# Kernel tuning notes

Hardware: AMD Instinct MI355X
Metric: run time of the kernel (lower is better)

The kernel has to match this reference:

```python
import jax, jax.numpy as jnp
import numpy as np

B, C, H, W = 4, 64, 64, 64
C8 = C // 8


def cl_attention(x, gamma):
    # DANet CAM-style channel attention: [B,C,H,W] -> [B,C,H,W]
    b, c, h, w = x.shape
    xf = x.reshape(b, c, h * w)                       # b c n
    energy = jnp.einsum('bcn,bdn->bcd', xf, xf)       # b c c
    energy = jnp.max(energy, axis=-1, keepdims=True) - energy
    attn = jax.nn.softmax(energy, axis=-1)
    out = jnp.einsum('bcd,bdn->bcn', attn, xf).reshape(b, c, h, w)
    return gamma * out + x


def setup_inputs() -> dict:
    key = jax.random.key(0)
    ks = jax.random.split(key, 8)
    s = 0.02
    return {
        'cnn_feat': jax.random.normal(ks[0], (B, C, H, W), jnp.float32),
        'vit_feat': jax.random.normal(ks[1], (B, C, H, W), jnp.float32),
        'Wq': jax.random.normal(ks[2], (C8, C), jnp.float32) * s,   # 1x1 conv kernel
        'bq': jnp.zeros((C8,), jnp.float32),
        'Wk': jax.random.normal(ks[3], (C8, C), jnp.float32) * s,
        'bk': jnp.zeros((C8,), jnp.float32),
        'Wv': jax.random.normal(ks[4], (C, C), jnp.float32) * s,
        'bv': jnp.zeros((C,), jnp.float32),
        'gamma': jnp.zeros((1,), jnp.float32),
        'gamma_cla_cnn': jnp.zeros((1,), jnp.float32),
        'gamma_cla_vit': jnp.zeros((1,), jnp.float32),
    }


def reference(cnn_feat, vit_feat, Wq, bq, Wk, bk, Wv, bv, gamma,
              gamma_cla_cnn, gamma_cla_vit):
    b, c, h, w = cnn_feat.shape
    n = h * w

    cnn_att = cl_attention(cnn_feat, gamma_cla_cnn)   # b c h w
    vit_att = cl_attention(vit_feat, gamma_cla_vit)   # b c h w

    # query: 1x1 conv -> view(b, C8, n) -> permute -> (b, n, C8)
    q = jnp.einsum('bchw,oc->bhwo', cnn_att, Wq).reshape(b, n, -1) + bq

    # vit: rearrange 'b c h w -> b (h w) c'
    vit_flat = vit_att.reshape(b, c, n).transpose(0, 2, 1)          # b n c
    k = vit_flat @ Wk.T + bk                                        # b n C8
    v = vit_flat @ Wv.T + bv                                        # b n C

    energy = jnp.einsum('bqd,bkd->bqk', q, k)                       # b n n
    attn = jax.nn.softmax(energy, axis=-1)
    out = jnp.einsum('bqk,bkc->bqc', attn, v)                       # b n c
    out = out.transpose(0, 2, 1).reshape(b, c, h, w)                # 'b (h w) c -> b c h w'
    return gamma * out + cnn_feat
```

## Files before the change

kernel.cpp:

```cpp
#include <hip/hip_runtime.h>
#include <hip/hip_bf16.h>

#define BSZ 4
#define CC 64
#define NN 4096
#define CN (CC*NN)
#define BCN (BSZ*CN)

typedef __attribute__((ext_vector_type(4))) float    f4v;
typedef __attribute__((ext_vector_type(4))) int      i4v;
typedef __attribute__((ext_vector_type(2))) int      i2v;
typedef __attribute__((ext_vector_type(2))) unsigned u2v;
typedef __attribute__((ext_vector_type(8))) short    s8v;

#define DPP_F(x_, ctrl_) __builtin_bit_cast(float, \
    __builtin_amdgcn_update_dpp(0, __builtin_bit_cast(int, (float)(x_)), (ctrl_), 0xf, 0xf, true))
#define QP_X1 0xB1

__device__ __forceinline__ unsigned pack_bf16(float lo, float hi) {
    unsigned l = __builtin_bit_cast(unsigned, lo);
    unsigned h = __builtin_bit_cast(unsigned, hi);
    return (h & 0xFFFF0000u) | (l >> 16);
}
__device__ __forceinline__ unsigned pack2(float lo, float hi) {
    float2 f2; f2.x = lo; f2.y = hi;
    __hip_bfloat162 h = __float22bfloat162_rn(f2);
    unsigned u;
    __builtin_memcpy(&u, &h, 4);
    return u;
}
__device__ __forceinline__ float blo(int d) {
    return __builtin_bit_cast(float, (unsigned)d << 16);
}
__device__ __forceinline__ float bhi(int d) {
    return __builtin_bit_cast(float, (unsigned)d & 0xFFFF0000u);
}

__global__ __launch_bounds__(256) void gram_k(const float* __restrict__ cnn,
                                              const float* __restrict__ vit,
                                              float* __restrict__ part) {
    __shared__ __align__(16) float sXT[128*68];
    int t = threadIdx.x;
    int blk = blockIdx.x;
    int ch = blk & 31, b = (blk >> 5) & 3, i2 = blk >> 7;
    const float* X = (i2 ? vit : cnn) + b * CN;
    int n0 = ch * 128;
#pragma unroll
    for (int j = 0; j < 8; j++) {
        int idx = t + j * 256;
        int c = idx >> 5, n4 = idx & 31;
        f4v val = *(const f4v*)&X[c * NN + n0 + n4 * 4];
        int base = (n4 * 4) * 68 + c;
        sXT[base]       = val[0];
        sXT[base + 68]  = val[1];
        sXT[base + 136] = val[2];
        sXT[base + 204] = val[3];
    }
    __syncthreads();
    int tc = (t & 15) * 4, td = (t >> 4) * 4;
    f4v acc[4];
#pragma unroll
    for (int i = 0; i < 4; i++) acc[i] = (f4v){0.f, 0.f, 0.f, 0.f};
#pragma unroll 4
    for (int k = 0; k < 128; k++) {
        f4v a  = *(const f4v*)&sXT[k * 68 + tc];
        f4v bb = *(const f4v*)&sXT[k * 68 + td];
#pragma unroll
        for (int i = 0; i < 4; i++) acc[i] += a[i] * bb;
    }
    float* dst = part + ch * 32768 + (i2 * 4 + b) * 4096;
#pragma unroll
    for (int i = 0; i < 4; i++) *(f4v*)&dst[(tc + i) * 64 + td] = acc[i];
}

__global__ void gred_k(const float* __restrict__ part, float* __restrict__ G) {
    int row = blockIdx.x;
    int d = threadIdx.x;
    float s = 0.f;
#pragma unroll 8
    for (int ch = 0; ch < 32; ch++) s += part[ch * 32768 + row * 64 + d];
    float mn = s;
#pragma unroll
    for (int off = 1; off < 64; off <<= 1) mn = fminf(mn, __shfl_xor(mn, off));
    float e = __expf(mn - s);
    float sm = e;
#pragma unroll
    for (int off = 1; off < 64; off <<= 1) sm += __shfl_xor(sm, off);
    G[row * 64 + d] = e / sm;
}

__global__ __launch_bounds__(256) void weff_k(const float* __restrict__ G,
                                              const float* __restrict__ Wq,
                                              const float* __restrict__ Wk,
                                              const float* __restrict__ Wv,
                                              const float* __restrict__ gcnn,
                                              const float* __restrict__ gvit,
                                              ushort* __restrict__ WeffB) {
    __shared__ float sA[8192];
    __shared__ float sWt[1024];
    int t = threadIdx.x;
    int b = blockIdx.x / 5, tile = blockIdx.x % 5;
    for (int i = t; i < 4096; i += 256) {
        sA[i]        = G[b * 4096 + i];
        sA[4096 + i] = G[(4 + b) * 4096 + i];
    }
    __syncthreads();
    float gc = *gcnn, gv = *gvit;
#pragma unroll
    for (int k = 0; k < 4; k++) {
        int idx = k * 256 + t;
        int r = idx >> 6, c = idx & 63;
        const float* Wrow; const float* A; float g;
        if (tile == 0) {
            if (r < 8) { Wrow = Wq + r * 64;       A = sA;        g = gc; }
            else       { Wrow = Wk + (r - 8) * 64; A = sA + 4096; g = gv; }
        } else         { Wrow = Wv + ((tile - 1) * 16 + r) * 64; A = sA + 4096; g = gv; }
        float s = 0.f;
#pragma unroll 8
        for (int d = 0; d < 64; d++) s += Wrow[d] * A[d * 64 + c];
        sWt[idx] = g * s + Wrow[c];
    }
    __syncthreads();
    if (t < 128) {
        int frag = t >> 6, lane = t & 63, m = lane & 15, q4 = lane >> 4;
        i4v o;
#pragma unroll
        for (int p = 0; p < 4; p++) {
            int c0 = frag * 32 + q4 * 8 + 2 * p;
            o[p] = (int)pack_bf16(sWt[m * 64 + c0], sWt[m * 64 + c0 + 1]);
        }
        *(i4v*)&WeffB[(size_t)(b * 10 + tile * 2 + frag) * 512 + lane * 8] = o;
    }
}

__global__ __launch_bounds__(256) void qkv_k(const float* __restrict__ cnn,
                                             const float* __restrict__ vit,
                                             const ushort* __restrict__ WeffB,
                                             const float* __restrict__ bq,
                                             const float* __restrict__ bk,
                                             const float* __restrict__ bv,
                                             ushort* __restrict__ qb, ushort* __restrict__ kb,
                                             ushort* __restrict__ vT) {
    int t = threadIdx.x;
    int b = blockIdx.x >> 6, n0 = (blockIdx.x & 63) * 64;
    int w = t >> 6, lane = t & 63, c15 = lane & 15, q4 = lane >> 4;
    int n = n0 + w * 16 + c15;
    const float LOG2E = 1.44269504f;

    s8v A[10];
    const ushort* WB = WeffB + (size_t)b * 5120 + lane * 8;
#pragma unroll
    for (int i = 0; i < 10; i++)
        A[i] = __builtin_bit_cast(s8v, *(const i4v*)(WB + (size_t)i * 512));

    s8v Bc[2], Bv[2];
#pragma unroll
    for (int f = 0; f < 2; f++) {
        i4v pc, pv;
#pragma unroll
        for (int p = 0; p < 4; p++) {
            int c0 = f * 32 + q4 * 8 + p * 2;
            size_t a0 = (size_t)b * CN + (size_t)c0 * NN + n;
            pc[p] = (int)pack_bf16(cnn[a0], cnn[a0 + NN]);
            pv[p] = (int)pack_bf16(vit[a0], vit[a0 + NN]);
        }
        Bc[f] = __builtin_bit_cast(s8v, pc);
        Bv[f] = __builtin_bit_cast(s8v, pv);
    }

    f4v acc = *(const f4v*)(bq + (q4 & 1) * 4);
    acc = __builtin_amdgcn_mfma_f32_16x16x32_bf16(A[0], Bc[0], acc, 0, 0, 0);
    acc = __builtin_amdgcn_mfma_f32_16x16x32_bf16(A[1], Bc[1], acc, 0, 0, 0);
    if (q4 < 2) {
        unsigned d0 = pack_bf16(acc[0] * LOG2E, acc[1] * LOG2E);
        unsigned d1 = pack_bf16(acc[2] * LOG2E, acc[3] * LOG2E);
        unsigned long long v = ((unsigned long long)d1 << 32) | d0;
        *(unsigned long long*)&qb[(size_t)(b * NN + n) * 8 + q4 * 4] = v;
    }
    acc = *(const f4v*)(bk + (q4 & 1) * 4);
    acc = __builtin_amdgcn_mfma_f32_16x16x32_bf16(A[0], Bv[0], acc, 0, 0, 0);
    acc = __builtin_amdgcn_mfma_f32_16x16x32_bf16(A[1], Bv[1], acc, 0, 0, 0);
    if (q4 >= 2) {
        unsigned d0 = pack_bf16(acc[0], acc[1]), d1 = pack_bf16(acc[2], acc[3]);
        unsigned long long v = ((unsigned long long)d1 << 32) | d0;
        *(unsigned long long*)&kb[(size_t)(b * NN + n) * 8 + (q4 - 2) * 4] = v;
    }
#pragma unroll
    for (int tile = 1; tile < 5; tile++) {
        acc = *(const f4v*)(bv + (tile - 1) * 16 + q4 * 4);
        acc = __builtin_amdgcn_mfma_f32_16x16x32_bf16(A[tile * 2],     Bv[0], acc, 0, 0, 0);
        acc = __builtin_amdgcn_mfma_f32_16x16x32_bf16(A[tile * 2 + 1], Bv[1], acc, 0, 0, 0);
#pragma unroll
        for (int r = 0; r < 4; r++) {
            float other = DPP_F(acc[r], QP_X1);
            unsigned pkd = (lane & 1) ? pack_bf16(other, acc[r])
                                      : pack_bf16(acc[r], other);
            if (!(lane & 1)) {
                int row = (tile - 1) * 16 + q4 * 4 + r;
                *(unsigned*)&vT[(size_t)(b * 64 + row) * NN + n] = pkd;
            }
        }
    }
}

__global__ __launch_bounds__(256, 2) void flash_k(const ushort* __restrict__ qb,
                                                  const ushort* __restrict__ kb,
                                                  const ushort* __restrict__ vT,
                                                  ushort* __restrict__ pOT,
                                                  float* __restrict__ pl) {
    __shared__ __align__(16) ushort Vlds[2 * 64 * 72];
    int t = threadIdx.x;
    int lane = t & 63, w = t >> 6;
    int c15 = lane & 15, q4 = lane >> 4;
    int blk = blockIdx.x;
    int s = blk >> 7, b = (blk >> 5) & 3, q0 = (blk & 31) * 128;

    s8v qB[2];
#pragma unroll
    for (int g = 0; g < 2; g++) {
        i4v qa = (i4v){0, 0, 0, 0};
        if (q4 == 0)
            qa = *(const i4v*)(qb + (size_t)(b * NN + q0 + w * 32 + g * 16 + c15) * 8);
        qB[g] = __builtin_bit_cast(s8v, qa);
    }

    f4v accO[2][4];
#pragma unroll
    for (int g = 0; g < 2; g++)
#pragma unroll
        for (int nt = 0; nt < 4; nt++) accO[g][nt] = (f4v){0.f, 0.f, 0.f, 0.f};
    float lacc[2] = {0.f, 0.f};

    const ushort* kbb = kb + (size_t)b * NN * 8 + (size_t)c15 * 8;

    int r = t >> 2, chk = t & 3;
    const ushort* vsrc = vT + (size_t)(b * 64 + r) * NN + chk * 16;
    int vdstoff = r * 72 + 32 * (chk >> 1) + 4 * (chk & 1);
    int vreadoff = c15 * 72 + 8 * q4;

    int kbase = s * 1024;
    i4v bk_cur[4];
#pragma unroll
    for (int nt = 0; nt < 4; nt++)
        bk_cur[nt] = *(const i4v*)(kbb + (size_t)(kbase + nt * 16) * 8);
    i4v v0 = *(const i4v*)(vsrc + kbase);
    i4v v1 = *(const i4v*)(vsrc + kbase + 8);

#pragma unroll 2
    for (int kt = 0; kt < 16; kt++) {
        int k0 = kbase + kt * 64;
        ushort* vd = Vlds + (kt & 1) * 4608 + vdstoff;
        *(i2v*)(vd + 0)  = (i2v){v0[0], v0[1]};
        *(i2v*)(vd + 8)  = (i2v){v0[2], v0[3]};
        *(i2v*)(vd + 16) = (i2v){v1[0], v1[1]};
        *(i2v*)(vd + 24) = (i2v){v1[2], v1[3]};
        __syncthreads();

        const ushort* vb = Vlds + (kt & 1) * 4608 + vreadoff;
        i4v vA[2][4];
#pragma unroll
        for (int F = 0; F < 2; F++)
#pragma unroll
            for (int nt = 0; nt < 4; nt++)
                vA[F][nt] = *(const i4v*)(vb + nt * 16 * 72 + 32 * F);

        i4v bk_nxt[4];
        if (kt < 15) {
            v0 = *(const i4v*)(vsrc + k0 + 64);
            v1 = *(const i4v*)(vsrc + k0 + 64 + 8);
#pragma unroll
            for (int nt = 0; nt < 4; nt++)
                bk_nxt[nt] = *(const i4v*)(kbb + (size_t)(k0 + 64 + nt * 16) * 8);
        }

        f4v z = (f4v){0.f, 0.f, 0.f, 0.f};
        f4v S[2][4];
#pragma unroll
        for (int g = 0; g < 2; g++)
#pragma unroll
            for (int nt = 0; nt < 4; nt++)
                S[g][nt] = __builtin_amdgcn_mfma_f32_16x16x32_bf16(
                    __builtin_bit_cast(s8v, bk_cur[nt]), qB[g], z, 0, 0, 0);

        s8v Bp[2][2];
#pragma unroll
        for (int g = 0; g < 2; g++) {
            f4v p[4];
            float ps = 0.f;
#pragma unroll
            for (int nt = 0; nt < 4; nt++)
#pragma unroll
                for (int rr = 0; rr < 4; rr++) {
                    p[nt][rr] = __builtin_amdgcn_exp2f(S[g][nt][rr]);
                    ps += p[nt][rr];
                }
#pragma unroll
            for (int F = 0; F < 2; F++) {
                i4v bp;
                bp[0] = (int)pack2(p[2 * F][0],     p[2 * F][1]);
                bp[1] = (int)pack2(p[2 * F][2],     p[2 * F][3]);
                bp[2] = (int)pack2(p[2 * F + 1][0], p[2 * F + 1][1]);
                bp[3] = (int)pack2(p[2 * F + 1][2], p[2 * F + 1][3]);
                Bp[g][F] = __builtin_bit_cast(s8v, bp);
            }
            lacc[g] += ps;
        }

        __builtin_amdgcn_s_setprio(1);
#pragma unroll
        for (int F = 0; F < 2; F++)
#pragma unroll
            for (int g = 0; g < 2; g++)
#pragma unroll
                for (int nt = 0; nt < 4; nt++)
                    accO[g][nt] =
                        __builtin_amdgcn_mfma_f32_16x16x32_bf16(
                            __builtin_bit_cast(s8v, vA[F][nt]), Bp[g][F],
                            accO[g][nt], 0, 0, 0);
        __builtin_amdgcn_s_setprio(0);

        if (kt < 15) {
#pragma unroll
            for (int nt = 0; nt < 4; nt++) bk_cur[nt] = bk_nxt[nt];
        }
    }

#pragma unroll
    for (int g = 0; g < 2; g++) {
        lacc[g] += __shfl_xor(lacc[g], 16);
        lacc[g] += __shfl_xor(lacc[g], 32);
    }

#pragma unroll
    for (int g = 0; g < 2; g++) {
        int qg = q0 + w * 32 + g * 16 + c15;
#pragma unroll
        for (int nt = 0; nt < 4; nt++) {
            int cg = nt * 4 + q4;
            u2v d;
            d[0] = pack2(accO[g][nt][0], accO[g][nt][1]);
            d[1] = pack2(accO[g][nt][2], accO[g][nt][3]);
            *(u2v*)&pOT[((size_t)((s * 4 + b) * 16 + cg) * NN + qg) * 4] = d;
        }
        if (q4 == 0)
            pl[(size_t)(s * 4 + b) * NN + qg] = lacc[g];
    }
}

__global__ __launch_bounds__(256) void comb_k(const ushort* __restrict__ pOT,
                                              const float* __restrict__ pl,
                                              const float* __restrict__ cnn,
                                              const float* __restrict__ gamma,
                                              float* __restrict__ out) {
    int t = threadIdx.x;
    int b = blockIdx.x >> 6, n0 = (blockIdx.x & 63) * 64;
    int nq = t & 15, cl = t >> 4;
    int n = n0 + nq * 4;
    f4v L = (f4v){0.f, 0.f, 0.f, 0.f};
#pragma unroll
    for (int s = 0; s < 4; s++)
        L += *(const f4v*)&pl[(size_t)(s * 4 + b) * NN + n];
    float g = *gamma;
    f4v rv;
#pragma unroll
    for (int j = 0; j < 4; j++) rv[j] = g / L[j];

    f4v Oc[4];
#pragma unroll
    for (int cc = 0; cc < 4; cc++) Oc[cc] = (f4v){0.f, 0.f, 0.f, 0.f};
#pragma unroll
    for (int s = 0; s < 4; s++) {
        const ushort* src = pOT + ((size_t)((s * 4 + b) * 16 + cl) * NN + n) * 4;
        i4v a  = *(const i4v*)src;
        i4v bb = *(const i4v*)(src + 8);
        Oc[0][0] += blo(a[0]);  Oc[1][0] += bhi(a[0]);
        Oc[2][0] += blo(a[1]);  Oc[3][0] += bhi(a[1]);
        Oc[0][1] += blo(a[2]);  Oc[1][1] += bhi(a[2]);
        Oc[2][1] += blo(a[3]);  Oc[3][1] += bhi(a[3]);
        Oc[0][2] += blo(bb[0]); Oc[1][2] += bhi(bb[0]);
        Oc[2][2] += blo(bb[1]); Oc[3][2] += bhi(bb[1]);
        Oc[0][3] += blo(bb[2]); Oc[1][3] += bhi(bb[2]);
        Oc[2][3] += blo(bb[3]); Oc[3][3] += bhi(bb[3]);
    }
#pragma unroll
    for (int cc = 0; cc < 4; cc++) {
        size_t gi = (size_t)(b * 64 + cl * 4 + cc) * NN + n;
        f4v cv = *(const f4v*)&cnn[gi];
        *(f4v*)&out[gi] = Oc[cc] * rv + cv;
    }
}

extern "C" void kernel_launch(void* const* d_in, const int* in_sizes, int n_in,
                              void* d_out, int out_size, void* d_ws, size_t ws_size,
                              hipStream_t stream) {
    const float* cnn  = (const float*)d_in[0];
    const float* vit  = (const float*)d_in[1];
    const float* Wq   = (const float*)d_in[2];
    const float* bq   = (const float*)d_in[3];
    const float* Wk   = (const float*)d_in[4];
    const float* bk   = (const float*)d_in[5];
    const float* Wv   = (const float*)d_in[6];
    const float* bv   = (const float*)d_in[7];
    const float* gam  = (const float*)d_in[8];
    const float* gcnn = (const float*)d_in[9];
    const float* gvit = (const float*)d_in[10];
    float* out = (float*)d_out;

    float* ws = (float*)d_ws;
    ushort* pOT   = (ushort*)ws;
    float*  part  = ws;
    float*  G     = ws + 8388608;
    ushort* WeffB = (ushort*)(ws + 8421376);
    ushort* qb    = (ushort*)(ws + 8431616);
    ushort* kb    = (ushort*)(ws + 8497152);
    ushort* vT    = (ushort*)(ws + 8562688);
    float*  pl    = ws + 9086976;

    gram_k <<<256, 256, 0, stream>>>(cnn, vit, part);
    gred_k <<<512, 64,  0, stream>>>(part, G);
    weff_k <<<20,  256, 0, stream>>>(G, Wq, Wk, Wv, gcnn, gvit, WeffB);
    qkv_k  <<<256, 256, 0, stream>>>(cnn, vit, WeffB, bq, bk, bv, qb, kb, vT);
    flash_k<<<512, 256, 0, stream>>>(qb, kb, vT, pOT, pl);
    comb_k <<<256, 256, 0, stream>>>(pOT, pl, cnn, gam, out);
}
```

Before: 126.6 us.

## Fuse split-K combine into flash kernel with in-block LDS reduction and prepacked V fragments

Drops the separate combine kernel and the bf16 partial-output and denominator buffers. Each block now handles 64 queries, and its four waves each cover a quarter of the keys. The waves reduce their partial outputs and softmax denominators through shared memory, then apply gamma and the residual add directly. qkv_k now writes V in MFMA-fragment order, so flashB loads V fragments straight from global memory with no LDS staging or per-iteration barriers. The cost is half as many blocks (256), more registers per wave for the larger accumulator set, and a multi-step LDS reduction at the end.

```diff
diff --git a/kernel.cpp b/kernel.cpp
--- a/kernel.cpp
+++ b/kernel.cpp
@@ -10,12 +10,7 @@
 typedef __attribute__((ext_vector_type(4))) float    f4v;
 typedef __attribute__((ext_vector_type(4))) int      i4v;
 typedef __attribute__((ext_vector_type(2))) int      i2v;
-typedef __attribute__((ext_vector_type(2))) unsigned u2v;
 typedef __attribute__((ext_vector_type(8))) short    s8v;
-
-#define DPP_F(x_, ctrl_) __builtin_bit_cast(float, \
-    __builtin_amdgcn_update_dpp(0, __builtin_bit_cast(int, (float)(x_)), (ctrl_), 0xf, 0xf, true))
-#define QP_X1 0xB1
 
 __device__ __forceinline__ unsigned pack_bf16(float lo, float hi) {
     unsigned l = __builtin_bit_cast(unsigned, lo);
@@ -28,12 +23,6 @@
     unsigned u;
     __builtin_memcpy(&u, &h, 4);
     return u;
-}
-__device__ __forceinline__ float blo(int d) {
-    return __builtin_bit_cast(float, (unsigned)d << 16);
-}
-__device__ __forceinline__ float bhi(int d) {
-    return __builtin_bit_cast(float, (unsigned)d & 0xFFFF0000u);
 }
 
 __global__ __launch_bounds__(256) void gram_k(const float* __restrict__ cnn,
@@ -140,9 +129,10 @@
                                              const float* __restrict__ bk,
                                              const float* __restrict__ bv,
                                              ushort* __restrict__ qb, ushort* __restrict__ kb,
-                                             ushort* __restrict__ vT) {
+                                             ushort* __restrict__ vF) {
+    __shared__ float vbuf[64 * 67];
     int t = threadIdx.x;
-    int b = blockIdx.x >> 6, n0 = (blockIdx.x & 63) * 64;
+    int b = blockIdx.x >> 6, ktg = blockIdx.x & 63, n0 = ktg * 64;
     int w = t >> 6, lane = t & 63, c15 = lane & 15, q4 = lane >> 4;
     int n = n0 + w * 16 + c15;
     const float LOG2E = 1.44269504f;
@@ -191,109 +181,104 @@
         acc = __builtin_amdgcn_mfma_f32_16x16x32_bf16(A[tile * 2],     Bv[0], acc, 0, 0, 0);
         acc = __builtin_amdgcn_mfma_f32_16x16x32_bf16(A[tile * 2 + 1], Bv[1], acc, 0, 0, 0);
 #pragma unroll
-        for (int r = 0; r < 4; r++) {
-            float other = DPP_F(acc[r], QP_X1);
-            unsigned pkd = (lane & 1) ? pack_bf16(other, acc[r])
-                                      : pack_bf16(acc[r], other);
-            if (!(lane & 1)) {
-                int row = (tile - 1) * 16 + q4 * 4 + r;
-                *(unsigned*)&vT[(size_t)(b * 64 + row) * NN + n] = pkd;
-            }
-        }
-    }
-}
-
-__global__ __launch_bounds__(256, 2) void flash_k(const ushort* __restrict__ qb,
-                                                  const ushort* __restrict__ kb,
-                                                  const ushort* __restrict__ vT,
-                                                  ushort* __restrict__ pOT,
-                                                  float* __restrict__ pl) {
-    __shared__ __align__(16) ushort Vlds[2 * 64 * 72];
+        for (int r = 0; r < 4; r++)
+            vbuf[((tile - 1) * 16 + q4 * 4 + r) * 67 + w * 16 + c15] = acc[r];
+    }
+    __syncthreads();
+    {
+        int nt = w, l = lane, q4f = q4, c15f = c15;
+#pragma unroll
+        for (int F = 0; F < 2; F++) {
+            float vv[8];
+#pragma unroll
+            for (int e = 0; e < 8; e++)
+                vv[e] = vbuf[(nt * 16 + c15f) * 67 + 32 * F + 16 * (e >> 2)
+                             + 4 * q4f + (e & 3)];
+            i4v o;
+#pragma unroll
+            for (int p = 0; p < 4; p++)
+                o[p] = (int)pack_bf16(vv[2 * p], vv[2 * p + 1]);
+            *(i4v*)&vF[((size_t)((b * 64 + ktg) * 8 + nt * 2 + F)) * 512 + l * 8] = o;
+        }
+    }
+}
+
+__global__ __launch_bounds__(256, 2) void flashB(
+        const ushort* __restrict__ qb, const ushort* __restrict__ kb,
+        const ushort* __restrict__ vF, const float* __restrict__ cnn,
+        const float* __restrict__ gamma, float* __restrict__ out) {
+    __shared__ __align__(16) float sO[2][64 * 68];
+    __shared__ float sL[4][64];
+    __shared__ float sRv[64];
+
     int t = threadIdx.x;
     int lane = t & 63, w = t >> 6;
     int c15 = lane & 15, q4 = lane >> 4;
     int blk = blockIdx.x;
-    int s = blk >> 7, b = (blk >> 5) & 3, q0 = (blk & 31) * 128;
-
-    s8v qB[2];
-#pragma unroll
-    for (int g = 0; g < 2; g++) {
+    int b = blk >> 6, q0 = (blk & 63) * 64;
+    float gm = *gamma;
+
+    s8v qB[4];
+#pragma unroll
+    for (int g = 0; g < 4; g++) {
         i4v qa = (i4v){0, 0, 0, 0};
         if (q4 == 0)
-            qa = *(const i4v*)(qb + (size_t)(b * NN + q0 + w * 32 + g * 16 + c15) * 8);
+            qa = *(const i4v*)(qb + (size_t)(b * NN + q0 + g * 16 + c15) * 8);
         qB[g] = __builtin_bit_cast(s8v, qa);
     }
 
-    f4v accO[2][4];
-#pragma unroll
-    for (int g = 0; g < 2; g++)
+    f4v accO[4][4];
+#pragma unroll
+    for (int g = 0; g < 4; g++)
 #pragma unroll
         for (int nt = 0; nt < 4; nt++) accO[g][nt] = (f4v){0.f, 0.f, 0.f, 0.f};
-    float lacc[2] = {0.f, 0.f};
+    float lacc[4] = {0.f, 0.f, 0.f, 0.f};
 
     const ushort* kbb = kb + (size_t)b * NN * 8 + (size_t)c15 * 8;
-
-    int r = t >> 2, chk = t & 3;
-    const ushort* vsrc = vT + (size_t)(b * 64 + r) * NN + chk * 16;
-    int vdstoff = r * 72 + 32 * (chk >> 1) + 4 * (chk & 1);
-    int vreadoff = c15 * 72 + 8 * q4;
-
-    int kbase = s * 1024;
-    i4v bk_cur[4];
+    const ushort* vfb = vF + (size_t)b * 64 * 8 * 512 + (size_t)lane * 8;
+    int kq = w * 1024;
+
+    i4v bkc[4];
 #pragma unroll
     for (int nt = 0; nt < 4; nt++)
-        bk_cur[nt] = *(const i4v*)(kbb + (size_t)(kbase + nt * 16) * 8);
-    i4v v0 = *(const i4v*)(vsrc + kbase);
-    i4v v1 = *(const i4v*)(vsrc + kbase + 8);
-
-#pragma unroll 2
+        bkc[nt] = *(const i4v*)(kbb + (size_t)(kq + nt * 16) * 8);
+
     for (int kt = 0; kt < 16; kt++) {
-        int k0 = kbase + kt * 64;
-        ushort* vd = Vlds + (kt & 1) * 4608 + vdstoff;
-        *(i2v*)(vd + 0)  = (i2v){v0[0], v0[1]};
-        *(i2v*)(vd + 8)  = (i2v){v0[2], v0[3]};
-        *(i2v*)(vd + 16) = (i2v){v1[0], v1[1]};
-        *(i2v*)(vd + 24) = (i2v){v1[2], v1[3]};
-        __syncthreads();
-
-        const ushort* vb = Vlds + (kt & 1) * 4608 + vreadoff;
+        int ktg = (kq >> 6) + kt;
         i4v vA[2][4];
 #pragma unroll
         for (int F = 0; F < 2; F++)
 #pragma unroll
             for (int nt = 0; nt < 4; nt++)
-                vA[F][nt] = *(const i4v*)(vb + nt * 16 * 72 + 32 * F);
-
-        i4v bk_nxt[4];
+                vA[F][nt] = *(const i4v*)(vfb +
+                    (size_t)(ktg * 8 + nt * 2 + F) * 512);
+        i4v bkn[4];
         if (kt < 15) {
-            v0 = *(const i4v*)(vsrc + k0 + 64);
-            v1 = *(const i4v*)(vsrc + k0 + 64 + 8);
-#pragma unroll
-            for (int nt = 0; nt < 4; nt++)
-                bk_nxt[nt] = *(const i4v*)(kbb + (size_t)(k0 + 64 + nt * 16) * 8);
-        }
-
-        f4v z = (f4v){0.f, 0.f, 0.f, 0.f};
-        f4v S[2][4];
-#pragma unroll
-        for (int g = 0; g < 2; g++)
-#pragma unroll
-            for (int nt = 0; nt < 4; nt++)
-                S[g][nt] = __builtin_amdgcn_mfma_f32_16x16x32_bf16(
-                    __builtin_bit_cast(s8v, bk_cur[nt]), qB[g], z, 0, 0, 0);
-
-        s8v Bp[2][2];
-#pragma unroll
-        for (int g = 0; g < 2; g++) {
+#pragma unroll
+            for (int nt = 0; nt < 4; nt++)
+                bkn[nt] = *(const i4v*)(kbb +
+                    (size_t)(kq + (kt + 1) * 64 + nt * 16) * 8);
+        }
+
+#pragma unroll
+        for (int g = 0; g < 4; g++) {
+            f4v z = (f4v){0.f, 0.f, 0.f, 0.f};
+            f4v S[4];
+#pragma unroll
+            for (int nt = 0; nt < 4; nt++)
+                S[nt] = __builtin_amdgcn_mfma_f32_16x16x32_bf16(
+                    __builtin_bit_cast(s8v, bkc[nt]), qB[g], z, 0, 0, 0);
             f4v p[4];
             float ps = 0.f;
 #pragma unroll
             for (int nt = 0; nt < 4; nt++)
 #pragma unroll
                 for (int rr = 0; rr < 4; rr++) {
-                    p[nt][rr] = __builtin_amdgcn_exp2f(S[g][nt][rr]);
+                    p[nt][rr] = __builtin_amdgcn_exp2f(S[nt][rr]);
                     ps += p[nt][rr];
                 }
+            lacc[g] += ps;
+            s8v Bp[2];
 #pragma unroll
             for (int F = 0; F < 2; F++) {
                 i4v bp;
@@ -301,92 +286,88 @@
                 bp[1] = (int)pack2(p[2 * F][2],     p[2 * F][3]);
                 bp[2] = (int)pack2(p[2 * F + 1][0], p[2 * F + 1][1]);
                 bp[3] = (int)pack2(p[2 * F + 1][2], p[2 * F + 1][3]);
-                Bp[g][F] = __builtin_bit_cast(s8v, bp);
+                Bp[F] = __builtin_bit_cast(s8v, bp);
             }
-            lacc[g] += ps;
-        }
-
-        __builtin_amdgcn_s_setprio(1);
-#pragma unroll
-        for (int F = 0; F < 2; F++)
-#pragma unroll
-            for (int g = 0; g < 2; g++)
+            __builtin_amdgcn_s_setprio(1);
+#pragma unroll
+            for (int F = 0; F < 2; F++)
 #pragma unroll
                 for (int nt = 0; nt < 4; nt++)
-                    accO[g][nt] =
-                        __builtin_amdgcn_mfma_f32_16x16x32_bf16(
-                            __builtin_bit_cast(s8v, vA[F][nt]), Bp[g][F],
-                            accO[g][nt], 0, 0, 0);
-        __builtin_amdgcn_s_setprio(0);
-
+                    accO[g][nt] = __builtin_amdgcn_mfma_f32_16x16x32_bf16(
+                        __builtin_bit_cast(s8v, vA[F][nt]), Bp[F],
+                        accO[g][nt], 0, 0, 0);
+            __builtin_amdgcn_s_setprio(0);
+        }
         if (kt < 15) {
 #pragma unroll
-            for (int nt = 0; nt < 4; nt++) bk_cur[nt] = bk_nxt[nt];
-        }
-    }
-
-#pragma unroll
-    for (int g = 0; g < 2; g++) {
+            for (int nt = 0; nt < 4; nt++) bkc[nt] = bkn[nt];
+        }
+    }
+
+#pragma unroll
+    for (int g = 0; g < 4; g++) {
         lacc[g] += __shfl_xor(lacc[g], 16);
         lacc[g] += __shfl_xor(lacc[g], 32);
-    }
-
-#pragma unroll
-    for (int g = 0; g < 2; g++) {
-        int qg = q0 + w * 32 + g * 16 + c15;
-#pragma unroll
-        for (int nt = 0; nt < 4; nt++) {
-            int cg = nt * 4 + q4;
-            u2v d;
-            d[0] = pack2(accO[g][nt][0], accO[g][nt][1]);
-            d[1] = pack2(accO[g][nt][2], accO[g][nt][3]);
-            *(u2v*)&pOT[((size_t)((s * 4 + b) * 16 + cg) * NN + qg) * 4] = d;
-        }
-        if (q4 == 0)
-            pl[(size_t)(s * 4 + b) * NN + qg] = lacc[g];
-    }
-}
-
-__global__ __launch_bounds__(256) void comb_k(const ushort* __restrict__ pOT,
-                                              const float* __restrict__ pl,
-                                              const float* __restrict__ cnn,
-                                              const float* __restrict__ gamma,
-                                              float* __restrict__ out) {
-    int t = threadIdx.x;
-    int b = blockIdx.x >> 6, n0 = (blockIdx.x & 63) * 64;
-    int nq = t & 15, cl = t >> 4;
-    int n = n0 + nq * 4;
-    f4v L = (f4v){0.f, 0.f, 0.f, 0.f};
-#pragma unroll
-    for (int s = 0; s < 4; s++)
-        L += *(const f4v*)&pl[(size_t)(s * 4 + b) * NN + n];
-    float g = *gamma;
-    f4v rv;
-#pragma unroll
-    for (int j = 0; j < 4; j++) rv[j] = g / L[j];
-
-    f4v Oc[4];
-#pragma unroll
-    for (int cc = 0; cc < 4; cc++) Oc[cc] = (f4v){0.f, 0.f, 0.f, 0.f};
-#pragma unroll
-    for (int s = 0; s < 4; s++) {
-        const ushort* src = pOT + ((size_t)((s * 4 + b) * 16 + cl) * NN + n) * 4;
-        i4v a  = *(const i4v*)src;
-        i4v bb = *(const i4v*)(src + 8);
-        Oc[0][0] += blo(a[0]);  Oc[1][0] += bhi(a[0]);
-        Oc[2][0] += blo(a[1]);  Oc[3][0] += bhi(a[1]);
-        Oc[0][1] += blo(a[2]);  Oc[1][1] += bhi(a[2]);
-        Oc[2][1] += blo(a[3]);  Oc[3][1] += bhi(a[3]);
-        Oc[0][2] += blo(bb[0]); Oc[1][2] += bhi(bb[0]);
-        Oc[2][2] += blo(bb[1]); Oc[3][2] += bhi(bb[1]);
-        Oc[0][3] += blo(bb[2]); Oc[1][3] += bhi(bb[2]);
-        Oc[2][3] += blo(bb[3]); Oc[3][3] += bhi(bb[3]);
-    }
-#pragma unroll
-    for (int cc = 0; cc < 4; cc++) {
-        size_t gi = (size_t)(b * 64 + cl * 4 + cc) * NN + n;
+        if (q4 == 0) sL[w][g * 16 + c15] = lacc[g];
+    }
+    if (w >= 2) {
+        float* s = sO[w - 2];
+#pragma unroll
+        for (int g = 0; g < 4; g++)
+#pragma unroll
+            for (int nt = 0; nt < 4; nt++)
+#pragma unroll
+                for (int rr = 0; rr < 4; rr++)
+                    s[(nt * 16 + q4 * 4 + rr) * 68 + g * 16 + c15] = accO[g][nt][rr];
+    }
+    __syncthreads();
+    if (w < 2) {
+        float* s = sO[w];
+#pragma unroll
+        for (int g = 0; g < 4; g++)
+#pragma unroll
+            for (int nt = 0; nt < 4; nt++)
+#pragma unroll
+                for (int rr = 0; rr < 4; rr++)
+                    accO[g][nt][rr] += s[(nt * 16 + q4 * 4 + rr) * 68 + g * 16 + c15];
+    }
+    if (w == 1) {
+        float* s = sO[1];
+#pragma unroll
+        for (int g = 0; g < 4; g++)
+#pragma unroll
+            for (int nt = 0; nt < 4; nt++)
+#pragma unroll
+                for (int rr = 0; rr < 4; rr++)
+                    s[(nt * 16 + q4 * 4 + rr) * 68 + g * 16 + c15] = accO[g][nt][rr];
+    }
+    if (w == 2) {
+        float Ls = sL[0][lane] + sL[1][lane] + sL[2][lane] + sL[3][lane];
+        sRv[lane] = gm / Ls;
+    }
+    __syncthreads();
+    if (w == 0) {
+        float* s1 = sO[1];
+        float* s0 = sO[0];
+#pragma unroll
+        for (int g = 0; g < 4; g++)
+#pragma unroll
+            for (int nt = 0; nt < 4; nt++)
+#pragma unroll
+                for (int rr = 0; rr < 4; rr++) {
+                    int off = (nt * 16 + q4 * 4 + rr) * 68 + g * 16 + c15;
+                    s0[off] = accO[g][nt][rr] + s1[off];
+                }
+    }
+    __syncthreads();
+#pragma unroll
+    for (int it = 0; it < 4; it++) {
+        int c = it * 16 + (t >> 4), l16 = t & 15, q = l16 * 4;
+        f4v o  = *(const f4v*)&sO[0][c * 68 + q];
+        f4v rv = *(const f4v*)&sRv[q];
+        size_t gi = (size_t)(b * 64 + c) * NN + q0 + q;
         f4v cv = *(const f4v*)&cnn[gi];
-        *(f4v*)&out[gi] = Oc[cc] * rv + cv;
+        *(f4v*)&out[gi] = o * rv + cv;
     }
 }
 
@@ -407,19 +388,16 @@
     float* out = (float*)d_out;
 
     float* ws = (float*)d_ws;
-    ushort* pOT   = (ushort*)ws;
     float*  part  = ws;
-    float*  G     = ws + 8388608;
-    ushort* WeffB = (ushort*)(ws + 8421376);
-    ushort* qb    = (ushort*)(ws + 8431616);
-    ushort* kb    = (ushort*)(ws + 8497152);
-    ushort* vT    = (ushort*)(ws + 8562688);
-    float*  pl    = ws + 9086976;
-
-    gram_k <<<256, 256, 0, stream>>>(cnn, vit, part);
-    gred_k <<<512, 64,  0, stream>>>(part, G);
-    weff_k <<<20,  256, 0, stream>>>(G, Wq, Wk, Wv, gcnn, gvit, WeffB);
-    qkv_k  <<<256, 256, 0, stream>>>(cnn, vit, WeffB, bq, bk, bv, qb, kb, vT);
-    flash_k<<<512, 256, 0, stream>>>(qb, kb, vT, pOT, pl);
-    comb_k <<<256, 256, 0, stream>>>(pOT, pl, cnn, gam, out);
-}
+    float*  G     = ws + 1048576;
+    ushort* WeffB = (ushort*)(ws + 1081344);
+    ushort* qb    = (ushort*)(ws + 1091584);
+    ushort* kb    = (ushort*)(ws + 1157120);
+    ushort* vF    = (ushort*)(ws + 1222656);
+
+    gram_k<<<256, 256, 0, stream>>>(cnn, vit, part);
+    gred_k<<<512, 64,  0, stream>>>(part, G);
+    weff_k<<<20,  256, 0, stream>>>(G, Wq, Wk, Wv, gcnn, gvit, WeffB);
+    qkv_k <<<256, 256, 0, stream>>>(cnn, vit, WeffB, bq, bk, bv, qb, kb, vF);
+    flashB<<<256, 256, 0, stream>>>(qb, kb, vF, cnn, gam, out);
+}
```

Measured after the change: 125.1 us. No clear change (-1.2%).
